# Kernel tuning notes

Measured on AMD Instinct MI355X. Metric: run time of the kernel, lower is better.

## Reference

```python
import jax, jax.numpy as jnp
import numpy as np

B, S, N, D, C, H = 256, 256, 128, 256, 512, 4  # batch, seq, mem_slots, mem_dim, controller_dim, heads
HD = D // H


def setup_inputs() -> dict:
    key = jax.random.key(0)
    ks = jax.random.split(key, 12)
    sc = 0.02
    p = lambda k, shape: (jax.random.normal(k, shape, jnp.float32) * sc)
    return {
        "input_seq": jax.random.normal(ks[0], (B, S, D), jnp.float32),
        "memory_init": jax.random.normal(ks[1], (N, D), jnp.float32) * (np.sqrt(6.0 / (N + D)) / np.sqrt(3.0)),
        # LSTM (torch gate order i, f, g, o)
        "W_ih": p(ks[2], (4 * C, D)), "W_hh": p(ks[3], (4 * C, C)),
        "b_ih": jnp.zeros((4 * C,), jnp.float32), "b_hh": jnp.zeros((4 * C,), jnp.float32),
        # heads
        "W_read": p(ks[4], (D, C)), "b_read": jnp.zeros((D,), jnp.float32),
        "W_write": p(ks[5], (2 * D, C)), "b_write": jnp.zeros((2 * D,), jnp.float32),
        "W_erase": p(ks[6], (D, C)), "b_erase": jnp.zeros((D,), jnp.float32),
        # MultiheadAttention packed in-proj (q,k,v) + out-proj
        "W_in": p(ks[7], (3 * D, D)), "b_in": jnp.zeros((3 * D,), jnp.float32),
        "W_out": p(ks[8], (D, D)), "b_out": jnp.zeros((D,), jnp.float32),
        # gates
        "W_rg": p(ks[9], (1, C)), "b_rg": jnp.zeros((1,), jnp.float32),
        "W_wg": p(ks[10], (1, C)), "b_wg": jnp.zeros((1,), jnp.float32),
    }


def reference(input_seq, memory_init, W_ih, W_hh, b_ih, b_hh,
              W_read, b_read, W_write, b_write, W_erase, b_erase,
              W_in, b_in, W_out, b_out, W_rg, b_rg, W_wg, b_wg):
    b, s, d = input_seq.shape
    Wq, Wk, Wv = jnp.split(W_in, 3, axis=0)
    bq, bk, bv = jnp.split(b_in, 3)
    inv_sqrt_hd = 1.0 / np.sqrt(HD)

    mem0 = jnp.broadcast_to(memory_init, (b,) + memory_init.shape)
    h0 = jnp.zeros((b, C), input_seq.dtype)
    c0 = jnp.zeros((b, C), input_seq.dtype)

    def step(carry, x_t):
        h, c, mem = carry  # h,c: [B,C]; mem: [B,N,D]
        # LSTM cell (torch gate order i,f,g,o)
        gates = x_t @ W_ih.T + b_ih + h @ W_hh.T + b_hh
        i, f, g, o = jnp.split(gates, 4, axis=-1)
        c = jax.nn.sigmoid(f) * c + jax.nn.sigmoid(i) * jnp.tanh(g)
        h = jax.nn.sigmoid(o) * jnp.tanh(c)
        # --- read: MHA(query=read_key, key=value=memory) ---
        rk = h @ W_read.T + b_read                      # [B,D]
        q = (rk @ Wq.T + bq).reshape(b, H, HD)          # [B,H,hd]
        k = (mem @ Wk.T + bk).reshape(b, -1, H, HD)     # [B,N,H,hd]
        v = (mem @ Wv.T + bv).reshape(b, -1, H, HD)
        scores = jnp.einsum('bhd,bnhd->bhn', q, k) * inv_sqrt_hd
        attn = jax.nn.softmax(scores, axis=-1)          # [B,H,N]
        ctx = jnp.einsum('bhn,bnhd->bhd', attn, v).reshape(b, d)
        read_out = ctx @ W_out.T + b_out
        read_gate = jax.nn.sigmoid(h @ W_rg.T + b_rg)   # [B,1]
        read = read_gate * read_out
        # --- write: erase/add ---
        wp = h @ W_write.T + b_write
        write_key, write_val = wp[:, :d], wp[:, d:]
        erase_vec = jax.nn.sigmoid(h @ W_erase.T + b_erase)  # [B,D]
        write_gate = jax.nn.sigmoid(h @ W_wg.T + b_wg)       # [B,1]
        wa = jax.nn.softmax(jnp.einsum('bd,bnd->bn', write_key, mem), axis=-1)  # [B,N]
        ew = wa[:, :, None]                                   # [B,N,1]
        mem = mem * (1.0 - ew * erase_vec[:, None, :]) + write_gate[:, None, :] * (ew * write_val[:, None, :])
        return (h, c, mem), x_t + read

    (hT, cT, memT), outs = jax.lax.scan(step, (h0, c0, mem0), jnp.swapaxes(input_seq, 0, 1))
    output_sequence = jnp.swapaxes(outs, 0, 1)  # [B,S,D]
    return output_sequence, memT
```

## Files before the change

kernel.cpp:

```cpp
#include <hip/hip_runtime.h>

#define S_LEN 256
#define B_SZ  256
#define N_MEM 128
#define D_DIM 256
#define C_DIM 512
#define NBLK  256
#define MSTR  260
#define AGENT __HIP_MEMORY_SCOPE_AGENT

typedef __bf16 bf16x8 __attribute__((ext_vector_type(8)));
typedef unsigned short ushort4v __attribute__((ext_vector_type(4)));
typedef float floatx4 __attribute__((ext_vector_type(4)));
typedef float floatx2 __attribute__((ext_vector_type(2)));

__device__ __forceinline__ unsigned short f2bf(float f){
  unsigned u = __float_as_uint(f);
  u += 0x7FFFu + ((u >> 16) & 1u);
  return (unsigned short)(u >> 16);
}
__device__ __forceinline__ float bf2f(unsigned short v){
  return __uint_as_float(((unsigned)v) << 16);
}
__device__ __forceinline__ float sigm(float x){ return 1.f/(1.f + __expf(-x)); }
__device__ __forceinline__ floatx4 mfma16(bf16x8 a, bf16x8 b, floatx4 c){
  return __builtin_amdgcn_mfma_f32_16x16x32_bf16(a, b, c, 0, 0, 0);
}

__device__ __forceinline__ unsigned ald32(const void* p){
  return __hip_atomic_load((const unsigned*)p, __ATOMIC_RELAXED, AGENT);
}
__device__ __forceinline__ void ast32(void* p, unsigned v){
  __hip_atomic_store((unsigned*)p, v, __ATOMIC_RELAXED, AGENT);
}
__device__ __forceinline__ void ast64(void* p, unsigned long long v){
  __hip_atomic_store((unsigned long long*)p, v, __ATOMIC_RELAXED, AGENT);
}
__device__ __forceinline__ void sst16(void* p, unsigned short v){
  asm volatile("global_store_short %0, %1, off sc1" :: "v"(p), "v"(v) : "memory");
}

struct V16 { floatx4 v0,v1,v2,v3,v4,v5,v6,v7,v8,v9,v10,v11,v12,v13,v14,v15; };
#define BC(xx) __builtin_bit_cast(bf16x8, xx)

__device__ __forceinline__ V16 cload16(const unsigned short* base){
  V16 r;
  asm volatile(
    "global_load_dwordx4 %0, %16, off sc1\n\t"
    "global_load_dwordx4 %1, %16, off offset:64 sc1\n\t"
    "global_load_dwordx4 %2, %16, off offset:128 sc1\n\t"
    "global_load_dwordx4 %3, %16, off offset:192 sc1\n\t"
    "global_load_dwordx4 %4, %16, off offset:256 sc1\n\t"
    "global_load_dwordx4 %5, %16, off offset:320 sc1\n\t"
    "global_load_dwordx4 %6, %16, off offset:384 sc1\n\t"
    "global_load_dwordx4 %7, %16, off offset:448 sc1\n\t"
    "global_load_dwordx4 %8, %16, off offset:512 sc1\n\t"
    "global_load_dwordx4 %9, %16, off offset:576 sc1\n\t"
    "global_load_dwordx4 %10, %16, off offset:640 sc1\n\t"
    "global_load_dwordx4 %11, %16, off offset:704 sc1\n\t"
    "global_load_dwordx4 %12, %16, off offset:768 sc1\n\t"
    "global_load_dwordx4 %13, %16, off offset:832 sc1\n\t"
    "global_load_dwordx4 %14, %16, off offset:896 sc1\n\t"
    "global_load_dwordx4 %15, %16, off offset:960 sc1\n\t"
    "s_waitcnt vmcnt(0)"
    : "=&v"(r.v0), "=&v"(r.v1), "=&v"(r.v2), "=&v"(r.v3),
      "=&v"(r.v4), "=&v"(r.v5), "=&v"(r.v6), "=&v"(r.v7),
      "=&v"(r.v8), "=&v"(r.v9), "=&v"(r.v10), "=&v"(r.v11),
      "=&v"(r.v12), "=&v"(r.v13), "=&v"(r.v14), "=&v"(r.v15)
    : "v"(base)
    : "memory");
  __builtin_amdgcn_sched_barrier(0);
  return r;
}

__device__ __forceinline__ void cload16_issue(const unsigned short* base, floatx4 r[16]){
  asm volatile(
    "global_load_dwordx4 %0, %16, off sc1\n\t"
    "global_load_dwordx4 %1, %16, off offset:64 sc1\n\t"
    "global_load_dwordx4 %2, %16, off offset:128 sc1\n\t"
    "global_load_dwordx4 %3, %16, off offset:192 sc1\n\t"
    "global_load_dwordx4 %4, %16, off offset:256 sc1\n\t"
    "global_load_dwordx4 %5, %16, off offset:320 sc1\n\t"
    "global_load_dwordx4 %6, %16, off offset:384 sc1\n\t"
    "global_load_dwordx4 %7, %16, off offset:448 sc1\n\t"
    "global_load_dwordx4 %8, %16, off offset:512 sc1\n\t"
    "global_load_dwordx4 %9, %16, off offset:576 sc1\n\t"
    "global_load_dwordx4 %10, %16, off offset:640 sc1\n\t"
    "global_load_dwordx4 %11, %16, off offset:704 sc1\n\t"
    "global_load_dwordx4 %12, %16, off offset:768 sc1\n\t"
    "global_load_dwordx4 %13, %16, off offset:832 sc1\n\t"
    "global_load_dwordx4 %14, %16, off offset:896 sc1\n\t"
    "global_load_dwordx4 %15, %16, off offset:960 sc1"
    : "=&v"(r[0]), "=&v"(r[1]), "=&v"(r[2]), "=&v"(r[3]),
      "=&v"(r[4]), "=&v"(r[5]), "=&v"(r[6]), "=&v"(r[7]),
      "=&v"(r[8]), "=&v"(r[9]), "=&v"(r[10]), "=&v"(r[11]),
      "=&v"(r[12]), "=&v"(r[13]), "=&v"(r[14]), "=&v"(r[15])
    : "v"(base)
    : "memory");
}
__device__ __forceinline__ void cwait16(floatx4 r[16]){
  asm volatile("s_waitcnt vmcnt(0)"
    : "+v"(r[0]), "+v"(r[1]), "+v"(r[2]), "+v"(r[3]),
      "+v"(r[4]), "+v"(r[5]), "+v"(r[6]), "+v"(r[7]),
      "+v"(r[8]), "+v"(r[9]), "+v"(r[10]), "+v"(r[11]),
      "+v"(r[12]), "+v"(r[13]), "+v"(r[14]), "+v"(r[15])
    :: "memory");
  __builtin_amdgcn_sched_barrier(0);
}


__global__ __launch_bounds__(256) void p0_xbf(const float* __restrict__ x,
                                              unsigned short* __restrict__ xbf){
  int idx = (blockIdx.x*256 + threadIdx.x)*4;
  floatx4 f = *(const floatx4*)(x + idx);
  ushort4v u;
  u[0]=f2bf(f[0]); u[1]=f2bf(f[1]); u[2]=f2bf(f[2]); u[3]=f2bf(f[3]);
  *(ushort4v*)(xbf + idx) = u;
}

__global__ __launch_bounds__(256) void p1_wg(const float* __restrict__ Wih,
                                             const float* __restrict__ Whh,
                                             unsigned short* __restrict__ Wg){
  int idx = blockIdx.x*256 + threadIdx.x;
  int n = idx / 768, k = idx - n*768;
  float v = (k < 256) ? Wih[n*256 + k] : Whh[n*512 + (k-256)];
  Wg[idx] = f2bf(v);
}

__global__ __launch_bounds__(256) void p2_T(const float* __restrict__ Win,
                                            const float* __restrict__ Wread,
                                            const float* __restrict__ bread,
                                            const float* __restrict__ bin,
                                            float* __restrict__ T, float* __restrict__ rq){
  if (blockIdx.x < 512){
    int idx = blockIdx.x*256 + threadIdx.x;
    int e = idx >> 9, cc = idx & 511;
    float acc = 0.f;
    for (int dp = 0; dp < 256; ++dp) acc += Win[e*256 + dp] * Wread[dp*512 + cc];
    T[idx] = acc;
  } else {
    int e = threadIdx.x;
    float acc = bin[e];
    for (int dp = 0; dp < 256; ++dp) acc += bread[dp] * Win[e*256 + dp];
    rq[e] = acc;
  }
}

__global__ __launch_bounds__(256) void p3_w2(const float* __restrict__ Win,
                                             const float* __restrict__ Wwrite,
                                             const float* __restrict__ Werase,
                                             const float* __restrict__ Wrg,
                                             const float* __restrict__ Wwg,
                                             const float* __restrict__ bwrite,
                                             const float* __restrict__ berase,
                                             const float* __restrict__ brg,
                                             const float* __restrict__ bwg,
                                             const float* __restrict__ T,
                                             const float* __restrict__ rq,
                                             unsigned short* __restrict__ W2,
                                             float* __restrict__ bias2){
  int bid = blockIdx.x;
  if (bid < 2048){
    int idx = bid*256 + threadIdx.x;
    int j = idx >> 9, cc = idx & 511;
    int h = j >> 8, d = j & 255;
    float acc = 0.f;
    const float* wk = Win + (256 + h*64)*256 + d;
    const float* tp = T + (h*64)*512 + cc;
    for (int i = 0; i < 64; ++i) acc += wk[i*256] * tp[i*512];
    W2[(size_t)j*512 + cc] = f2bf(acc);
  } else if (bid < 2048 + 1568){
    int idx = (bid - 2048)*256 + threadIdx.x;
    int r = idx >> 9, cc = idx & 511;
    float v;
    if      (r < 512) v = Wwrite[r*512 + cc];
    else if (r < 768) v = Werase[(r-512)*512 + cc];
    else if (r == 768) v = Wrg[cc];
    else if (r == 769) v = Wwg[cc];
    else v = 0.f;
    W2[(size_t)(1024 + r)*512 + cc] = f2bf(v);
  } else {
    int j = (bid - 2048 - 1568)*256 + threadIdx.x;
    if (j >= 1808) return;
    float v;
    if (j < 1024){
      int h = j >> 8, d = j & 255;
      float acc = 0.f;
      for (int i = 0; i < 64; ++i) acc += rq[h*64+i] * Win[(256 + h*64 + i)*256 + d];
      v = acc;
    }
    else if (j < 1536) v = bwrite[j - 1024];
    else if (j < 1792) v = berase[j - 1536];
    else if (j == 1792) v = brg[0];
    else if (j == 1793) v = bwg[0];
    else v = 0.f;
    bias2[j] = v;
  }
}

__global__ __launch_bounds__(256) void p4_fold(const float* __restrict__ Win,
                                               const float* __restrict__ Wout,
                                               const float* __restrict__ bout,
                                               const float* __restrict__ bin,
                                               unsigned short* __restrict__ Fold,
                                               float* __restrict__ bout2){
  if (blockIdx.x < 1024){
    int idx = blockIdx.x*256 + threadIdx.x;
    int dp = idx >> 10, j = idx & 1023;
    int h = j & 3, d = j >> 2;
    float acc = 0.f;
    const float* wv = Win + (512 + h*64)*256 + d;
    const float* wo = Wout + dp*256 + h*64;
    for (int i = 0; i < 64; ++i) acc += wv[i*256] * wo[i];
    Fold[(size_t)dp*1024 + j] = f2bf(acc);
  } else {
    int dp = threadIdx.x;
    float acc = bout[dp];
    for (int e = 0; e < 256; ++e) acc += Wout[dp*256 + e] * bin[512 + e];
    bout2[dp] = acc;
  }
}

__global__ __launch_bounds__(256) void p5_init(const float* __restrict__ bih,
                                               const float* __restrict__ bhh,
                                               float* __restrict__ biasg,
                                               float* __restrict__ c,
                                               unsigned short* __restrict__ h0){
  int idx = blockIdx.x*256 + threadIdx.x;
  c[idx] = 0.f; h0[idx] = 0;
  if (idx < 2048) biasg[idx] = bih[idx] + bhh[idx];
}

__device__ __forceinline__ void gbarg(unsigned* cnt, unsigned nb){
  __syncthreads();
  if (threadIdx.x == 0){
    __hip_atomic_fetch_add(cnt, 1u, __ATOMIC_RELAXED, AGENT);
    while (__hip_atomic_load(cnt, __ATOMIC_RELAXED, AGENT) < nb*16u)
      __builtin_amdgcn_s_sleep(1);
  }
  __builtin_amdgcn_sched_barrier(0);
  __syncthreads();
}


__device__ __forceinline__ void do_readout(int mt, int dt, int t,
                                           const unsigned short* __restrict__ mctx,
                                           const unsigned short* __restrict__ Fold,
                                           const float* __restrict__ rgb,
                                           const float* __restrict__ bout2,
                                           const float* __restrict__ x,
                                           float* __restrict__ out, int lane){
  const int lm = lane & 15, lk = (lane >> 4) * 8;
  const unsigned short* ap = mctx + (size_t)(mt*16 + lm)*1024 + lk;
  const unsigned short* bp = Fold + (size_t)(dt*16 + lm)*1024 + lk;
  const int r0 = mt*16 + ((lane >> 4) << 2);
  float rg0 = __uint_as_float(ald32(&rgb[r0]));
  float rg1 = __uint_as_float(ald32(&rgb[r0+1]));
  float rg2 = __uint_as_float(ald32(&rgb[r0+2]));
  float rg3 = __uint_as_float(ald32(&rgb[r0+3]));
  V16 a0 = cload16(ap);
  V16 a1 = cload16(ap + 512);
  const bf16x8 av[16] = {BC(a0.v0),BC(a0.v1),BC(a0.v2),BC(a0.v3),BC(a0.v4),BC(a0.v5),BC(a0.v6),BC(a0.v7),
                         BC(a0.v8),BC(a0.v9),BC(a0.v10),BC(a0.v11),BC(a0.v12),BC(a0.v13),BC(a0.v14),BC(a0.v15)};
  const bf16x8 bv[16] = {BC(a1.v0),BC(a1.v1),BC(a1.v2),BC(a1.v3),BC(a1.v4),BC(a1.v5),BC(a1.v6),BC(a1.v7),
                         BC(a1.v8),BC(a1.v9),BC(a1.v10),BC(a1.v11),BC(a1.v12),BC(a1.v13),BC(a1.v14),BC(a1.v15)};
  floatx4 acc = {0,0,0,0};
  #pragma unroll
  for (int kt = 0; kt < 16; ++kt)
    acc = mfma16(av[kt], *(const bf16x8*)(bp + kt*32), acc);
  #pragma unroll
  for (int kt = 0; kt < 16; ++kt)
    acc = mfma16(bv[kt], *(const bf16x8*)(bp + 512 + kt*32), acc);
  const int dp = dt*16 + lm;
  const float bo = bout2[dp];
  const float rg[4] = {rg0, rg1, rg2, rg3};
  #pragma unroll
  for (int q = 0; q < 4; ++q){
    const int bb = r0 + q;
    const size_t oi = ((size_t)bb * S_LEN + (t-1)) * D_DIM + dp;
    out[oi] = x[oi] + rg[q] * (acc[q] + bo);
  }
}

__global__ __launch_bounds__(512, 2) void kmain(
    const float* __restrict__ x,
    const unsigned short* __restrict__ xbf,
    const unsigned short* __restrict__ Wg,
    const float* __restrict__ biasg,
    const unsigned short* __restrict__ W2, const float* __restrict__ bias2,
    const unsigned short* __restrict__ Fold, const float* __restrict__ bout2,
    float* __restrict__ cbuf,
    unsigned short* __restrict__ h0buf, unsigned short* __restrict__ h1buf,
    unsigned short* __restrict__ projB, unsigned short* __restrict__ mctx,
    float* __restrict__ rgbuf, const float* __restrict__ mem0,
    float* __restrict__ memT, float* __restrict__ out,
    unsigned* __restrict__ barcnt)
{
  const int bid = blockIdx.x, tid = threadIdx.x;
  const int lane = tid & 63, wave = tid >> 6;
  const int lm = lane & 15, lk = (lane >> 4) * 8;

  __shared__ float memL[128][MSTR];
  __shared__ float scU[5][512];
  __shared__ float qkW[5][256];
  __shared__ float er[256];
  __shared__ float wvs[256];
  __shared__ float attT[128][8];
  __shared__ float wgS;
  float (*ga)[16][32] = (float (*)[16][32])&scU[0][0];
  floatx4* mpart = (floatx4*)&scU[0][0];

  const int r = bid >> 4, uc = bid & 15, u0 = uc*32;
  unsigned* gcnt = barcnt + r*16;

  for (int i = tid; i < 32768; i += 512) memL[i >> 8][i & 255] = mem0[i];

  unsigned nbar = 0;
  const unsigned short* hr = h0buf;
  unsigned short* hw = h1buf;
  const int g = wave >> 1, colh = wave & 1;
  const int row = r*16 + lm;
  const int slot = uc*8 + wave;

  floatx4 hq[16];
  bf16x8 xfr[8];
  cload16_issue(hr + (size_t)row*C_DIM + lk, hq);
  {
    const unsigned short* ax = xbf + ((size_t)row*S_LEN + 0)*D_DIM + lk;
    #pragma unroll
    for (int kt = 0; kt < 8; ++kt) xfr[kt] = *(const bf16x8*)(ax + kt*32);
  }

  for (int t = 0; t < S_LEN; ++t){
    {
      const unsigned short* wb = Wg + (size_t)(g*512 + u0 + colh*16 + lm)*768 + lk;
      cwait16(hq);
      floatx4 acc = {0,0,0,0};
      #pragma unroll
      for (int kt = 0; kt < 8; ++kt)
        acc = mfma16(xfr[kt], *(const bf16x8*)(wb + kt*32), acc);
      #pragma unroll
      for (int kt = 0; kt < 16; ++kt)
        acc = mfma16(BC(hq[kt]), *(const bf16x8*)(wb + 256 + kt*32), acc);
      const int rr0 = (lane >> 4) << 2;
      #pragma unroll
      for (int q = 0; q < 4; ++q) ga[g][rr0+q][colh*16 + lm] = acc[q];
      __syncthreads();
      if (tid < 256){
        const int ri = tid >> 4, cp = (tid & 15) * 2;
        const int b = r*16 + ri, u = u0 + cp;
        floatx2 bg0 = *(const floatx2*)&biasg[u];
        floatx2 bg1 = *(const floatx2*)&biasg[512 + u];
        floatx2 bg2 = *(const floatx2*)&biasg[1024 + u];
        floatx2 bg3 = *(const floatx2*)&biasg[1536 + u];
        const float gi0 = ga[0][ri][cp]   + bg0[0];
        const float gf0 = ga[1][ri][cp]   + bg1[0];
        const float gg0 = ga[2][ri][cp]   + bg2[0];
        const float go0 = ga[3][ri][cp]   + bg3[0];
        const float gi1 = ga[0][ri][cp+1] + bg0[1];
        const float gf1 = ga[1][ri][cp+1] + bg1[1];
        const float gg1 = ga[2][ri][cp+1] + bg2[1];
        const float go1 = ga[3][ri][cp+1] + bg3[1];
        const int ci2 = b*512 + u;
        floatx2 cv = *(const floatx2*)&cbuf[ci2];
        const float cn0 = sigm(gf0) * cv[0] + sigm(gi0) * tanhf(gg0);
        const float cn1 = sigm(gf1) * cv[1] + sigm(gi1) * tanhf(gg1);
        floatx2 cw; cw[0] = cn0; cw[1] = cn1;
        *(floatx2*)&cbuf[ci2] = cw;
        const unsigned hv2 = (unsigned)f2bf(sigm(go0) * tanhf(cn0))
                           | ((unsigned)f2bf(sigm(go1) * tanhf(cn1)) << 16);
        ast32((unsigned*)hw + (ci2 >> 1), hv2);
      }
    }
    gbarg(gcnt, ++nbar);
    {
      const float* rgprev = rgbuf + ((t-1)&1)*256;
      float* rgcur = rgbuf + (t&1)*256;
      for (int j = slot; j < 129; j += 128){
        if (j < 113){
          const int nt = j;
          const unsigned short* ap = hw + (size_t)(r*16 + lm)*512 + lk;
          const unsigned short* bp = W2 + (size_t)(nt*16 + lm)*512 + lk;
          V16 av16 = cload16(ap);
          const bf16x8 av[16] = {BC(av16.v0),BC(av16.v1),BC(av16.v2),BC(av16.v3),BC(av16.v4),BC(av16.v5),BC(av16.v6),BC(av16.v7),
                                 BC(av16.v8),BC(av16.v9),BC(av16.v10),BC(av16.v11),BC(av16.v12),BC(av16.v13),BC(av16.v14),BC(av16.v15)};
          floatx4 acc = {0,0,0,0};
          #pragma unroll
          for (int kt = 0; kt < 16; ++kt)
            acc = mfma16(av[kt], *(const bf16x8*)(bp + kt*32), acc);
          const int r0 = r*16 + ((lane >> 4) << 2);
          const int cc = nt*16 + lm;
          const float bv = bias2[cc];
          const bool sg = (cc >= 1536 && cc < 1794);
          #pragma unroll
          for (int q = 0; q < 4; ++q){
            float v = acc[q] + bv;
            if (sg) v = sigm(v);
            sst16(&projB[(size_t)(r0 + q)*1808 + cc], f2bf(v));
            if (cc == 1792) ast32(&rgcur[r0 + q], __float_as_uint(v));
          }
        } else if (t >= 1){
          do_readout(r, j - 113, t, mctx, Fold, rgprev, bout2, x, out, lane);
        }
      }
    }
    gbarg(gcnt, ++nbar);
    {
      const unsigned* p32 = (const unsigned*)(projB + (size_t)bid*1808);
      for (int i = tid; i < 904; i += 512){
        unsigned u = ald32(p32 + i);
        float f0 = bf2f((unsigned short)(u & 0xFFFFu));
        float f1 = bf2f((unsigned short)(u >> 16));
        int j = i*2;
        if (j < 1024){ qkW[j>>8][j&255] = f0; qkW[j>>8][(j&255)+1] = f1; }
        else if (j < 1280){ qkW[4][j-1024] = f0; qkW[4][j-1023] = f1; }
        else if (j < 1536){ wvs[j-1280] = f0; wvs[j-1279] = f1; }
        else if (j < 1792){ er[j-1536] = f0; er[j-1535] = f1; }
        else { wgS = f1; }
      }
      __syncthreads();
      const float wgv = wgS;
      {
        const int n = tid & 127, quarter = tid >> 7, db = quarter*64;
        const float* mr = &memL[n][db];
        floatx4 A0={0,0,0,0},A1={0,0,0,0},A2={0,0,0,0},A3={0,0,0,0},A4={0,0,0,0};
        #pragma unroll 4
        for (int i = 0; i < 64; i += 4){
          floatx4 m4 = *(const floatx4*)(mr + i);
          floatx4 q0 = *(const floatx4*)&qkW[0][db+i];
          floatx4 q1 = *(const floatx4*)&qkW[1][db+i];
          floatx4 q2 = *(const floatx4*)&qkW[2][db+i];
          floatx4 q3 = *(const floatx4*)&qkW[3][db+i];
          floatx4 qw = *(const floatx4*)&qkW[4][db+i];
          A0 += m4*q0; A1 += m4*q1; A2 += m4*q2; A3 += m4*q3; A4 += m4*qw;
        }
        scU[0][tid] = A0[0]+A0[1]+A0[2]+A0[3];
        scU[1][tid] = A1[0]+A1[1]+A1[2]+A1[3];
        scU[2][tid] = A2[0]+A2[1]+A2[2]+A2[3];
        scU[3][tid] = A3[0]+A3[1]+A3[2]+A3[3];
        scU[4][tid] = A4[0]+A4[1]+A4[2]+A4[3];
      }
      __syncthreads();
      if (tid < 128){
        #pragma unroll
        for (int j = 0; j < 5; ++j){
          float v = scU[j][tid] + scU[j][tid+128] + scU[j][tid+256] + scU[j][tid+384];
          scU[j][tid] = (j < 4) ? v * 0.125f : v;
        }
      }
      __syncthreads();
      {
        const int w = tid >> 6, l = tid & 63;
        if (w < 5){
          const int j = w;
          float v0 = scU[j][l], v1 = scU[j][l + 64];
          float mx = fmaxf(v0, v1);
          #pragma unroll
          for (int off = 32; off; off >>= 1) mx = fmaxf(mx, __shfl_xor(mx, off));
          float e0 = __expf(v0 - mx), e1 = __expf(v1 - mx);
          float sm = e0 + e1;
          #pragma unroll
          for (int off = 32; off; off >>= 1) sm += __shfl_xor(sm, off);
          float inv = 1.f / sm;
          attT[l][j] = e0 * inv; attT[l + 64][j] = e1 * inv;
        }
      }
      __syncthreads();
      floatx4 M = {0,0,0,0};
      {
        const int d = tid & 255, n0 = (tid >> 8) * 64;
        #pragma unroll 4
        for (int n = n0; n < n0 + 64; ++n){
          floatx4 a4 = *(const floatx4*)&attT[n][0];
          float m = memL[n][d];
          M += a4 * m;
        }
        if (tid >= 256) mpart[d] = M;
      }
      __syncthreads();
      if (tid < 256){
        floatx4 M2 = M + mpart[tid];
        const unsigned lo = (unsigned)f2bf(M2[0]) | ((unsigned)f2bf(M2[1]) << 16);
        const unsigned hi = (unsigned)f2bf(M2[2]) | ((unsigned)f2bf(M2[3]) << 16);
        ast64((unsigned long long*)(mctx + (size_t)bid*1024) + tid,
              (unsigned long long)lo | ((unsigned long long)hi << 32));
      }
      __syncthreads();
      {
        const int d4 = (tid & 63)*4, nw = tid >> 6;
        floatx4 er4 = *(const floatx4*)&er[d4];
        floatx4 wv4 = *(const floatx4*)&wvs[d4];
        #pragma unroll 4
        for (int k = 0; k < 16; ++k){
          const int n = nw + k*8;
          const float a = attT[n][4];
          floatx4 m = *(const floatx4*)&memL[n][d4];
          m = m * (1.f - a*er4) + (wgv*a) * wv4;
          *(floatx4*)&memL[n][d4] = m;
        }
      }
      {
        const int tn = (t+1 < S_LEN) ? t+1 : t;
        const unsigned short* ax = xbf + ((size_t)row*S_LEN + tn)*D_DIM + lk;
        #pragma unroll
        for (int kt = 0; kt < 8; ++kt) xfr[kt] = *(const bf16x8*)(ax + kt*32);
        cload16_issue(hw + (size_t)row*C_DIM + lk, hq);
      }
    }
    unsigned short* tmp = (unsigned short*)hr; hr = hw; hw = tmp;
  }
  gbarg(gcnt, ++nbar);
  if (wave == 0)
    do_readout(r, uc, S_LEN, mctx, Fold, rgbuf + ((S_LEN-1)&1)*256, bout2, x, out, lane);
  for (int i = tid; i < 32768; i += 512)
    memT[(size_t)bid * 32768 + i] = memL[i >> 8][i & 255];
}


extern "C" void kernel_launch(void* const* d_in, const int* in_sizes, int n_in,
                              void* d_out, int out_size, void* d_ws, size_t ws_size,
                              hipStream_t stream){
  const float* x      = (const float*)d_in[0];
  const float* mem0   = (const float*)d_in[1];
  const float* Wih    = (const float*)d_in[2];
  const float* Whh    = (const float*)d_in[3];
  const float* bih    = (const float*)d_in[4];
  const float* bhh    = (const float*)d_in[5];
  const float* Wread  = (const float*)d_in[6];
  const float* bread  = (const float*)d_in[7];
  const float* Wwrite = (const float*)d_in[8];
  const float* bwrite = (const float*)d_in[9];
  const float* Werase = (const float*)d_in[10];
  const float* berase = (const float*)d_in[11];
  const float* Win    = (const float*)d_in[12];
  const float* bin    = (const float*)d_in[13];
  const float* Wout   = (const float*)d_in[14];
  const float* bout   = (const float*)d_in[15];
  const float* Wrg    = (const float*)d_in[16];
  const float* brg    = (const float*)d_in[17];
  const float* Wwg    = (const float*)d_in[18];
  const float* bwg    = (const float*)d_in[19];
  float* out = (float*)d_out;
  float* memT = out + (size_t)B_SZ * S_LEN * D_DIM;

  char* ws = (char*)d_ws;
  size_t off = 0;
  auto alloc = [&](size_t bytes) -> void* {
    void* p = ws + off; off += (bytes + 511) & ~(size_t)511; return p;
  };
  unsigned short* xbf  = (unsigned short*)alloc((size_t)B_SZ*S_LEN*D_DIM*2);
  unsigned short* Wg   = (unsigned short*)alloc((size_t)2048*768*2);
  unsigned short* W2   = (unsigned short*)alloc((size_t)1808*512*2);
  unsigned short* Fold = (unsigned short*)alloc((size_t)256*1024*2);
  float* T     = (float*)alloc((size_t)256*512*4);
  float* rq    = (float*)alloc(256*4);
  float* bias2 = (float*)alloc(1808*4);
  float* bout2 = (float*)alloc(256*4);
  float* biasg = (float*)alloc(2048*4);
  float* cbuf  = (float*)alloc((size_t)256*512*4);
  unsigned short* h0 = (unsigned short*)alloc((size_t)256*512*2);
  unsigned short* h1 = (unsigned short*)alloc((size_t)256*512*2);
  unsigned short* projB = (unsigned short*)alloc((size_t)256*1808*2);
  unsigned short* mctx = (unsigned short*)alloc((size_t)256*1024*2);
  float* rgbuf = (float*)alloc(512*4);
  unsigned* barcnt = (unsigned*)alloc(4096);
  (void)ws_size; (void)in_sizes; (void)n_in; (void)out_size;

  (void)hipMemsetAsync(barcnt, 0, 4096, stream);
  p0_xbf <<<16384, 256, 0, stream>>>(x, xbf);
  p1_wg  <<<6144, 256, 0, stream>>>(Wih, Whh, Wg);
  p2_T   <<<513,  256, 0, stream>>>(Win, Wread, bread, bin, T, rq);
  p3_w2  <<<3624, 256, 0, stream>>>(Win, Wwrite, Werase, Wrg, Wwg, bwrite, berase, brg, bwg, T, rq, W2, bias2);
  p4_fold<<<1025, 256, 0, stream>>>(Win, Wout, bout, bin, Fold, bout2);
  p5_init<<<512,  256, 0, stream>>>(bih, bhh, biasg, cbuf, h0);

  kmain<<<NBLK, 512, 0, stream>>>(x, xbf, Wg, biasg, W2, bias2, Fold, bout2,
                                  cbuf, h0, h1, projB, mctx, rgbuf, mem0, memT, out, barcnt);
}
```

Before: 8.915 ms.

## Fuse memory-context reduction into erase/add update and rebalance projection slots

The attention-weighted memory context (mctx) is now accumulated inside the erase/add memory update loop, using shuffle reductions. This removes a separate pass over shared memory, a partial-sum exchange and a block barrier. The read and write gate scalars are now computed per block from a staged copy of h, instead of in a 113th MFMA projection tile. That leaves exactly 128 work slots (112 projection tiles plus 16 readouts), so no wave has to run a second iteration. The read-gate buffer is single-buffered, projB loads are widened to 64 bits, and the launch-bounds occupancy hint is dropped, which may change register allocation.

```diff
diff --git a/kernel.cpp b/kernel.cpp
--- a/kernel.cpp
+++ b/kernel.cpp
@@ -7,6 +7,7 @@
 #define C_DIM 512
 #define NBLK  256
 #define MSTR  260
+#define PROJS 1792
 #define AGENT __HIP_MEMORY_SCOPE_AGENT
 
 typedef __bf16 bf16x8 __attribute__((ext_vector_type(8)));
@@ -29,6 +30,9 @@
 
 __device__ __forceinline__ unsigned ald32(const void* p){
   return __hip_atomic_load((const unsigned*)p, __ATOMIC_RELAXED, AGENT);
+}
+__device__ __forceinline__ unsigned long long ald64(const void* p){
+  return __hip_atomic_load((const unsigned long long*)p, __ATOMIC_RELAXED, AGENT);
 }
 __device__ __forceinline__ void ast32(void* p, unsigned v){
   __hip_atomic_store((unsigned*)p, v, __ATOMIC_RELAXED, AGENT);
@@ -231,11 +235,11 @@
   if (idx < 2048) biasg[idx] = bih[idx] + bhh[idx];
 }
 
-__device__ __forceinline__ void gbarg(unsigned* cnt, unsigned nb){
+__device__ __forceinline__ void gbarg(unsigned* cnt, unsigned target){
   __syncthreads();
   if (threadIdx.x == 0){
     __hip_atomic_fetch_add(cnt, 1u, __ATOMIC_RELAXED, AGENT);
-    while (__hip_atomic_load(cnt, __ATOMIC_RELAXED, AGENT) < nb*16u)
+    while (__hip_atomic_load(cnt, __ATOMIC_RELAXED, AGENT) < target)
       __builtin_amdgcn_s_sleep(1);
   }
   __builtin_amdgcn_sched_barrier(0);
@@ -254,10 +258,10 @@
   const unsigned short* ap = mctx + (size_t)(mt*16 + lm)*1024 + lk;
   const unsigned short* bp = Fold + (size_t)(dt*16 + lm)*1024 + lk;
   const int r0 = mt*16 + ((lane >> 4) << 2);
-  float rg0 = __uint_as_float(ald32(&rgb[r0]));
-  float rg1 = __uint_as_float(ald32(&rgb[r0+1]));
-  float rg2 = __uint_as_float(ald32(&rgb[r0+2]));
-  float rg3 = __uint_as_float(ald32(&rgb[r0+3]));
+  const float rg0 = __uint_as_float(ald32(&rgb[r0]));
+  const float rg1 = __uint_as_float(ald32(&rgb[r0+1]));
+  const float rg2 = __uint_as_float(ald32(&rgb[r0+2]));
+  const float rg3 = __uint_as_float(ald32(&rgb[r0+3]));
   V16 a0 = cload16(ap);
   V16 a1 = cload16(ap + 512);
   const bf16x8 av[16] = {BC(a0.v0),BC(a0.v1),BC(a0.v2),BC(a0.v3),BC(a0.v4),BC(a0.v5),BC(a0.v6),BC(a0.v7),
@@ -282,7 +286,7 @@
   }
 }
 
-__global__ __launch_bounds__(512, 2) void kmain(
+__global__ __launch_bounds__(512) void kmain(
     const float* __restrict__ x,
     const unsigned short* __restrict__ xbf,
     const unsigned short* __restrict__ Wg,
@@ -306,9 +310,9 @@
   __shared__ float er[256];
   __shared__ float wvs[256];
   __shared__ float attT[128][8];
+  __shared__ float hL[512];
   __shared__ float wgS;
   float (*ga)[16][32] = (float (*)[16][32])&scU[0][0];
-  floatx4* mpart = (floatx4*)&scU[0][0];
 
   const int r = bid >> 4, uc = bid & 15, u0 = uc*32;
   unsigned* gcnt = barcnt + r*16;
@@ -372,54 +376,73 @@
         ast32((unsigned*)hw + (ci2 >> 1), hv2);
       }
     }
-    gbarg(gcnt, ++nbar);
+    gbarg(gcnt, (++nbar)*16u);
     {
-      const float* rgprev = rgbuf + ((t-1)&1)*256;
-      float* rgcur = rgbuf + (t&1)*256;
-      for (int j = slot; j < 129; j += 128){
-        if (j < 113){
-          const int nt = j;
-          const unsigned short* ap = hw + (size_t)(r*16 + lm)*512 + lk;
-          const unsigned short* bp = W2 + (size_t)(nt*16 + lm)*512 + lk;
-          V16 av16 = cload16(ap);
-          const bf16x8 av[16] = {BC(av16.v0),BC(av16.v1),BC(av16.v2),BC(av16.v3),BC(av16.v4),BC(av16.v5),BC(av16.v6),BC(av16.v7),
-                                 BC(av16.v8),BC(av16.v9),BC(av16.v10),BC(av16.v11),BC(av16.v12),BC(av16.v13),BC(av16.v14),BC(av16.v15)};
-          floatx4 acc = {0,0,0,0};
-          #pragma unroll
-          for (int kt = 0; kt < 16; ++kt)
-            acc = mfma16(av[kt], *(const bf16x8*)(bp + kt*32), acc);
-          const int r0 = r*16 + ((lane >> 4) << 2);
-          const int cc = nt*16 + lm;
-          const float bv = bias2[cc];
-          const bool sg = (cc >= 1536 && cc < 1794);
-          #pragma unroll
-          for (int q = 0; q < 4; ++q){
-            float v = acc[q] + bv;
-            if (sg) v = sigm(v);
-            sst16(&projB[(size_t)(r0 + q)*1808 + cc], f2bf(v));
-            if (cc == 1792) ast32(&rgcur[r0 + q], __float_as_uint(v));
-          }
-        } else if (t >= 1){
-          do_readout(r, j - 113, t, mctx, Fold, rgprev, bout2, x, out, lane);
-        }
+      if (slot < 112){
+        const int nt = slot;
+        const unsigned short* ap = hw + (size_t)(r*16 + lm)*512 + lk;
+        const unsigned short* bp = W2 + (size_t)(nt*16 + lm)*512 + lk;
+        V16 av16 = cload16(ap);
+        const bf16x8 av[16] = {BC(av16.v0),BC(av16.v1),BC(av16.v2),BC(av16.v3),BC(av16.v4),BC(av16.v5),BC(av16.v6),BC(av16.v7),
+                               BC(av16.v8),BC(av16.v9),BC(av16.v10),BC(av16.v11),BC(av16.v12),BC(av16.v13),BC(av16.v14),BC(av16.v15)};
+        floatx4 acc = {0,0,0,0};
+        #pragma unroll
+        for (int kt = 0; kt < 16; ++kt)
+          acc = mfma16(av[kt], *(const bf16x8*)(bp + kt*32), acc);
+        const int r0 = r*16 + ((lane >> 4) << 2);
+        const int cc = nt*16 + lm;
+        const float bv = bias2[cc];
+        const bool sg = (cc >= 1536);
+        #pragma unroll
+        for (int q = 0; q < 4; ++q){
+          float v = acc[q] + bv;
+          if (sg) v = sigm(v);
+          sst16(&projB[(size_t)(r0 + q)*PROJS + cc], f2bf(v));
+        }
+      } else if (t >= 1){
+        do_readout(r, slot - 112, t, mctx, Fold, rgbuf, bout2, x, out, lane);
       }
     }
-    gbarg(gcnt, ++nbar);
+    gbarg(gcnt, (++nbar)*16u);
     {
-      const unsigned* p32 = (const unsigned*)(projB + (size_t)bid*1808);
-      for (int i = tid; i < 904; i += 512){
-        unsigned u = ald32(p32 + i);
-        float f0 = bf2f((unsigned short)(u & 0xFFFFu));
-        float f1 = bf2f((unsigned short)(u >> 16));
-        int j = i*2;
-        if (j < 1024){ qkW[j>>8][j&255] = f0; qkW[j>>8][(j&255)+1] = f1; }
-        else if (j < 1280){ qkW[4][j-1024] = f0; qkW[4][j-1023] = f1; }
-        else if (j < 1536){ wvs[j-1280] = f0; wvs[j-1279] = f1; }
-        else if (j < 1792){ er[j-1536] = f0; er[j-1535] = f1; }
-        else { wgS = f1; }
+      const unsigned long long* p64 = (const unsigned long long*)(projB + (size_t)bid*PROJS);
+      if (tid < 448){
+        unsigned long long u2 = ald64(p64 + tid);
+        float e0 = bf2f((unsigned short)(u2 & 0xFFFFu));
+        float e1 = bf2f((unsigned short)((u2 >> 16) & 0xFFFFu));
+        float e2 = bf2f((unsigned short)((u2 >> 32) & 0xFFFFu));
+        float e3 = bf2f((unsigned short)(u2 >> 48));
+        const int j = tid*4;
+        if (j < 1024){ float* q = &qkW[j>>8][j&255]; q[0]=e0; q[1]=e1; q[2]=e2; q[3]=e3; }
+        else if (j < 1280){ float* q = &qkW[4][j-1024]; q[0]=e0; q[1]=e1; q[2]=e2; q[3]=e3; }
+        else if (j < 1536){ float* q = &wvs[j-1280]; q[0]=e0; q[1]=e1; q[2]=e2; q[3]=e3; }
+        else { float* q = &er[j-1536]; q[0]=e0; q[1]=e1; q[2]=e2; q[3]=e3; }
+      } else {
+        const int i = tid - 448;
+        const unsigned long long* h64 = (const unsigned long long*)(hw + (size_t)bid*C_DIM);
+        unsigned long long a = ald64(h64 + 2*i), b = ald64(h64 + 2*i + 1);
+        float* q = &hL[i*8];
+        q[0]=bf2f((unsigned short)(a & 0xFFFFu)); q[1]=bf2f((unsigned short)((a>>16)&0xFFFFu));
+        q[2]=bf2f((unsigned short)((a>>32)&0xFFFFu)); q[3]=bf2f((unsigned short)(a>>48));
+        q[4]=bf2f((unsigned short)(b & 0xFFFFu)); q[5]=bf2f((unsigned short)((b>>16)&0xFFFFu));
+        q[6]=bf2f((unsigned short)((b>>32)&0xFFFFu)); q[7]=bf2f((unsigned short)(b>>48));
       }
       __syncthreads();
-      const float wgv = wgS;
+      if (wave >= 6){
+        const int rowW = 1792 + (wave - 6);
+        const unsigned short* wrow = W2 + (size_t)rowW*512 + lane*8;
+        const float* hp = &hL[lane*8];
+        float s = 0.f;
+        #pragma unroll
+        for (int c = 0; c < 8; ++c) s += hp[c] * bf2f(wrow[c]);
+        #pragma unroll
+        for (int off = 32; off; off >>= 1) s += __shfl_xor(s, off);
+        if (lane == 0){
+          const float v = sigm(s + bias2[rowW]);
+          if (wave == 6) ast32(&rgbuf[bid], __float_as_uint(v));
+          else wgS = v;
+        }
+      }
       {
         const int n = tid & 127, quarter = tid >> 7, db = quarter*64;
         const float* mr = &memL[n][db];
@@ -466,37 +489,41 @@
         }
       }
       __syncthreads();
-      floatx4 M = {0,0,0,0};
       {
-        const int d = tid & 255, n0 = (tid >> 8) * 64;
-        #pragma unroll 4
-        for (int n = n0; n < n0 + 64; ++n){
-          floatx4 a4 = *(const floatx4*)&attT[n][0];
-          float m = memL[n][d];
-          M += a4 * m;
-        }
-        if (tid >= 256) mpart[d] = M;
-      }
-      __syncthreads();
-      if (tid < 256){
-        floatx4 M2 = M + mpart[tid];
-        const unsigned lo = (unsigned)f2bf(M2[0]) | ((unsigned)f2bf(M2[1]) << 16);
-        const unsigned hi = (unsigned)f2bf(M2[2]) | ((unsigned)f2bf(M2[3]) << 16);
-        ast64((unsigned long long*)(mctx + (size_t)bid*1024) + tid,
-              (unsigned long long)lo | ((unsigned long long)hi << 32));
-      }
-      __syncthreads();
-      {
-        const int d4 = (tid & 63)*4, nw = tid >> 6;
+        const float wgv = wgS;
+        const int dlow = lane & 7, ng = lane >> 3;
+        const int d4 = (wave*8 + dlow)*4;
         floatx4 er4 = *(const floatx4*)&er[d4];
         floatx4 wv4 = *(const floatx4*)&wvs[d4];
+        floatx4 A0={0,0,0,0},A1={0,0,0,0},A2={0,0,0,0},A3={0,0,0,0};
         #pragma unroll 4
         for (int k = 0; k < 16; ++k){
-          const int n = nw + k*8;
-          const float a = attT[n][4];
+          const int n = ng + k*8;
           floatx4 m = *(const floatx4*)&memL[n][d4];
-          m = m * (1.f - a*er4) + (wgv*a) * wv4;
+          floatx4 a4 = *(const floatx4*)&attT[n][0];
+          const float aw = attT[n][4];
+          A0 += a4[0]*m; A1 += a4[1]*m; A2 += a4[2]*m; A3 += a4[3]*m;
+          m = m * (1.f - aw*er4) + (wgv*aw) * wv4;
           *(floatx4*)&memL[n][d4] = m;
+        }
+        #pragma unroll
+        for (int off = 8; off <= 32; off <<= 1){
+          #pragma unroll
+          for (int c = 0; c < 4; ++c){
+            A0[c] += __shfl_xor(A0[c], off);
+            A1[c] += __shfl_xor(A1[c], off);
+            A2[c] += __shfl_xor(A2[c], off);
+            A3[c] += __shfl_xor(A3[c], off);
+          }
+        }
+        if (ng == 0){
+          unsigned long long* mrow = (unsigned long long*)(mctx + (size_t)bid*1024);
+          #pragma unroll
+          for (int dd = 0; dd < 4; ++dd){
+            const unsigned lo = (unsigned)f2bf(A0[dd]) | ((unsigned)f2bf(A1[dd]) << 16);
+            const unsigned hi = (unsigned)f2bf(A2[dd]) | ((unsigned)f2bf(A3[dd]) << 16);
+            ast64(mrow + d4 + dd, (unsigned long long)lo | ((unsigned long long)hi << 32));
+          }
         }
       }
       {
@@ -509,9 +536,9 @@
     }
     unsigned short* tmp = (unsigned short*)hr; hr = hw; hw = tmp;
   }
-  gbarg(gcnt, ++nbar);
+  gbarg(gcnt, (++nbar)*16u);
   if (wave == 0)
-    do_readout(r, uc, S_LEN, mctx, Fold, rgbuf + ((S_LEN-1)&1)*256, bout2, x, out, lane);
+    do_readout(r, uc, S_LEN, mctx, Fold, rgbuf, bout2, x, out, lane);
   for (int i = tid; i < 32768; i += 512)
     memT[(size_t)bid * 32768 + i] = memL[i >> 8][i & 255];
 }
@@ -560,9 +587,9 @@
   float* cbuf  = (float*)alloc((size_t)256*512*4);
   unsigned short* h0 = (unsigned short*)alloc((size_t)256*512*2);
   unsigned short* h1 = (unsigned short*)alloc((size_t)256*512*2);
-  unsigned short* projB = (unsigned short*)alloc((size_t)256*1808*2);
+  unsigned short* projB = (unsigned short*)alloc((size_t)256*PROJS*2);
   unsigned short* mctx = (unsigned short*)alloc((size_t)256*1024*2);
-  float* rgbuf = (float*)alloc(512*4);
+  float* rgbuf = (float*)alloc(256*4);
   unsigned* barcnt = (unsigned*)alloc(4096);
   (void)ws_size; (void)in_sizes; (void)n_in; (void)out_size;
 
```

Measured after the change: 8.960 ms. Within noise of the previous version (+0.5%).
